# Optimization experiments

Hardware: AMD Instinct MI355X
Metric: run time of the kernel (lower is better)

## Reference

```python
import jax, jax.numpy as jnp
import numpy as np

N_NODES = 100000
N_EDGES = 20000
NNZ = 1600000
D_IN = 128
D_OUT = 128


def setup_inputs() -> dict:
    key = jax.random.key(0)
    k1, k2, k3, k4, k5 = jax.random.split(key, 5)
    x_0 = jax.random.normal(k1, (N_NODES, D_IN), dtype=jnp.float32)
    # Kaiming-uniform-ish linear params
    W = jax.random.normal(k2, (D_OUT, D_IN), dtype=jnp.float32) * (1.0 / np.sqrt(D_IN))
    b = jax.random.normal(k3, (D_OUT,), dtype=jnp.float32) * 0.01
    # COO nonzeros of incidence_1 [n_nodes, n_edges]
    node_idx = jax.random.randint(k4, (NNZ,), 0, N_NODES, dtype=jnp.int32)
    edge_idx = jax.random.randint(k5, (NNZ,), 0, N_EDGES, dtype=jnp.int32)
    return {"x_0": x_0, "W": W, "b": b, "node_idx": node_idx, "edge_idx": edge_idx}


def reference(x_0, W, b, node_idx, edge_idx):
    # Linear transform: h = x_0 @ W^T + b  -> [n_nodes, out_channels]
    h = jnp.einsum('nd,od->no', x_0, W) + b
    # Hop 1 (e_aggr='sum'): m_0_1[e] = sum_{n in edge e} h[n]   (B_1^T @ h)
    m_0_1 = jax.ops.segment_sum(h[node_idx], edge_idx, num_segments=N_EDGES)
    # Hop 2 (v_aggr='mean'): m_1_0[n] = mean_{e ni n} m_0_1[e]  (B_1 @ m_0_1, row-mean)
    msg_sum = jax.ops.segment_sum(m_0_1[edge_idx], node_idx, num_segments=N_NODES)
    deg = jax.ops.segment_sum(jnp.ones((node_idx.shape[0],), dtype=h.dtype),
                              node_idx, num_segments=N_NODES)
    m_1_0 = msg_sum / jnp.maximum(deg, 1.0)[:, None]  # empty rows -> 0, as torch reduce='mean'
    return h + m_1_0
```

## Files before the change

kernel.cpp:

```cpp
#include <hip/hip_runtime.h>
#include <hip/hip_bf16.h>
#include <stddef.h>

#define N_NODES 100000
#define N_EDGES 20000
#define NNZ     1600000
#define DIM     128

#define NCH     128
#define CHUNK   (NNZ / NCH)

#define EHIST_NB  NCH
#define NHIST_B0  EHIST_NB
#define GEMM_B0   (NHIST_B0 + NCH)
#define GEMM_NB   391
#define P1_NB     (GEMM_B0 + GEMM_NB)

#define EBL 79
#define NBL 391

typedef short          bf16x8 __attribute__((ext_vector_type(8)));
typedef unsigned short u16x8  __attribute__((ext_vector_type(8)));
typedef float          f32x4  __attribute__((ext_vector_type(4)));
typedef float          f32x8  __attribute__((ext_vector_type(8)));

__device__ __forceinline__ unsigned short f2bf(float f) {
  union { float f; unsigned u; } c; c.f = f;
  unsigned r = c.u + 0x7FFFu + ((c.u >> 16) & 1u);
  return (unsigned short)(r >> 16);
}

__device__ __forceinline__ f32x8 bf2f8(u16x8 v) {
  f32x8 r;
  #pragma unroll
  for (int i = 0; i < 8; ++i) {
    union { unsigned u; float f; } c; c.u = ((unsigned)v[i]) << 16;
    r[i] = c.f;
  }
  return r;
}

__global__ void convw_kernel(const float* __restrict__ W, unsigned short* __restrict__ Wb) {
  int i = blockIdx.x * 256 + threadIdx.x;
  if (i < DIM * DIM) Wb[i] = f2bf(W[i]);
}

__global__ __launch_bounds__(1024, 8) void p1_kernel(
    const float* __restrict__ x, const unsigned short* __restrict__ Wb,
    const float* __restrict__ bias, unsigned short* __restrict__ hb,
    const int* __restrict__ ni, const int* __restrict__ ei,
    unsigned short* __restrict__ bhE16, unsigned short* __restrict__ locE,
    unsigned char* __restrict__ bhN, unsigned char* __restrict__ locN) {
  __shared__ unsigned smem[12500];
  const int bid = blockIdx.x;

  if (bid < EHIST_NB) {
    const int cb = bid;
    for (int k = threadIdx.x; k < 10000; k += 1024) smem[k] = 0u;
    __syncthreads();
    const int base = cb * CHUNK;
    for (int i = base + threadIdx.x; i < base + CHUNK; i += 1024) {
      int e = ei[i];
      const int word  = e >> 1;
      const int shift = (e & 1) * 16;
      unsigned old = atomicAdd(&smem[word], 1u << shift);
      locE[i] = (unsigned short)((old >> shift) & 0xFFFFu);
    }
    __syncthreads();
    unsigned short* dst = bhE16 + (size_t)cb * N_EDGES;
    for (int e = threadIdx.x; e < N_EDGES; e += 1024)
      dst[e] = (unsigned short)((smem[e >> 1] >> ((e & 1) * 16)) & 0xFFFFu);
  } else if (bid < GEMM_B0) {
    const int cb = bid - NHIST_B0;
    for (int k = threadIdx.x; k < 12500; k += 1024) smem[k] = 0u;
    __syncthreads();
    const int base = cb * CHUNK;
    for (int i = base + threadIdx.x; i < base + CHUNK; i += 1024) {
      int n = ni[i];
      const int word  = n >> 3;
      const int shift = (n & 7) * 4;
      unsigned old = atomicAdd(&smem[word], 1u << shift);
      locN[i] = (unsigned char)((old >> shift) & 15u);
    }
    __syncthreads();
    unsigned char* dst = bhN + (size_t)cb * N_NODES;
    for (int k = threadIdx.x; k < N_NODES; k += 1024)
      dst[k] = (unsigned char)((smem[k >> 3] >> ((k & 7) * 4)) & 15u);
  } else {
    const int wid = threadIdx.x >> 6;
    const int l   = threadIdx.x & 63;
    const int n0  = ((bid - GEMM_B0) * 16 + wid) * 16;
    if (n0 >= N_NODES) return;
    const int r  = l & 15;
    const int kg = l >> 4;

    bf16x8 a[4];
    {
      const float* xr = x + (size_t)(n0 + r) * DIM + kg * 8;
      #pragma unroll
      for (int kc = 0; kc < 4; ++kc) {
        const float4* p = reinterpret_cast<const float4*>(xr + kc * 32);
        float4 f0 = p[0], f1 = p[1];
        bf16x8 av;
        av[0]=(short)f2bf(f0.x); av[1]=(short)f2bf(f0.y); av[2]=(short)f2bf(f0.z); av[3]=(short)f2bf(f0.w);
        av[4]=(short)f2bf(f1.x); av[5]=(short)f2bf(f1.y); av[6]=(short)f2bf(f1.z); av[7]=(short)f2bf(f1.w);
        a[kc] = av;
      }
    }

    f32x4 acc[8];
    #pragma unroll
    for (int ot = 0; ot < 8; ++ot) acc[ot] = (f32x4){0.f, 0.f, 0.f, 0.f};

    #pragma unroll
    for (int ot = 0; ot < 8; ++ot) {
      const unsigned short* wr = Wb + (size_t)(r * 8 + ot) * DIM + kg * 8;
      #pragma unroll
      for (int kc = 0; kc < 4; ++kc) {
        bf16x8 bfrag = *reinterpret_cast<const bf16x8*>(wr + kc * 32);
        acc[ot] = __builtin_amdgcn_mfma_f32_16x16x32_bf16(a[kc], bfrag, acc[ot], 0, 0, 0);
      }
    }

    float bv[8];
    {
      const float4* bp = reinterpret_cast<const float4*>(bias + r * 8);
      float4 b0 = bp[0], b1 = bp[1];
      bv[0]=b0.x; bv[1]=b0.y; bv[2]=b0.z; bv[3]=b0.w;
      bv[4]=b1.x; bv[5]=b1.y; bv[6]=b1.z; bv[7]=b1.w;
    }

    #pragma unroll
    for (int j = 0; j < 4; ++j) {
      const int row = kg * 4 + j;
      u16x8 hv;
      #pragma unroll
      for (int ot = 0; ot < 8; ++ot) hv[ot] = f2bf(acc[ot][j] + bv[ot]);
      *reinterpret_cast<u16x8*>(&hb[(size_t)(n0 + row) * DIM + r * 8]) = hv;
    }
  }
}

__global__ __launch_bounds__(256) void scansA_kernel(
    unsigned short* __restrict__ bhE16, unsigned char* __restrict__ bhN,
    int* __restrict__ off_e, int* __restrict__ off_n,
    int* __restrict__ ebs, int* __restrict__ nbs) {
  __shared__ int lds[256];
  const int tx  = threadIdx.x;
  const int bid = blockIdx.x;
  int v;
  if (bid < EBL) {
    const int e = bid * 256 + tx;
    v = 0;
    if (e < N_EDGES) {
      unsigned short* p = bhE16 + e;
      int s = 0;
      #pragma unroll 8
      for (int b = 0; b < NCH; ++b) {
        int t = p[(size_t)b * N_EDGES];
        p[(size_t)b * N_EDGES] = (unsigned short)s;
        s += t;
      }
      v = s;
    }
  } else {
    const int k = (bid - EBL) * 256 + tx;
    v = 0;
    if (k < N_NODES) {
      unsigned char* p = bhN + k;
      int s = 0;
      #pragma unroll 8
      for (int b = 0; b < NCH; ++b) {
        int t = p[(size_t)b * N_NODES];
        p[(size_t)b * N_NODES] = (unsigned char)s;
        s += t;
      }
      v = s;
    }
  }
  int xv = v;
  lds[tx] = xv;
  __syncthreads();
  for (int off = 1; off < 256; off <<= 1) {
    int t = (tx >= off) ? lds[tx - off] : 0;
    __syncthreads();
    xv += t;
    lds[tx] = xv;
    __syncthreads();
  }
  if (bid < EBL) {
    const int e = bid * 256 + tx;
    if (e < N_EDGES) off_e[e] = xv - v;
    if (tx == 255) ebs[bid] = xv;
  } else {
    const int k = (bid - EBL) * 256 + tx;
    if (k < N_NODES) off_n[k] = xv - v;
    if (tx == 255) nbs[bid - EBL] = xv;
  }
}

__global__ __launch_bounds__(512) void scansB_kernel(int* __restrict__ ebs,
                                                     int* __restrict__ nbs) {
  __shared__ int lds[512];
  const int tx = threadIdx.x;
  int* a = (blockIdx.x == 0) ? ebs : nbs;
  const int m = (blockIdx.x == 0) ? EBL : NBL;
  int v = (tx < m) ? a[tx] : 0;
  int xv = v;
  lds[tx] = xv;
  __syncthreads();
  for (int off = 1; off < 512; off <<= 1) {
    int t = (tx >= off) ? lds[tx - off] : 0;
    __syncthreads();
    xv += t;
    lds[tx] = xv;
    __syncthreads();
  }
  if (tx < m) a[tx] = xv - v;
}

__global__ __launch_bounds__(256) void scansC_kernel(
    int* __restrict__ off_e, int* __restrict__ off_n,
    const int* __restrict__ ebs, const int* __restrict__ nbs) {
  const int tx  = threadIdx.x;
  const int bid = blockIdx.x;
  if (bid < EBL) {
    const int e = bid * 256 + tx;
    if (e < N_EDGES) off_e[e] += ebs[bid];
  } else {
    const int k = (bid - EBL) * 256 + tx;
    if (k < N_NODES) off_n[k] += nbs[bid - EBL];
  }
}

__global__ void scatter_kernel(const int* __restrict__ ni, const int* __restrict__ ei,
                               const int* __restrict__ off_n, const int* __restrict__ off_e,
                               const unsigned short* __restrict__ bhE16,
                               const unsigned char* __restrict__ bhN,
                               const unsigned short* __restrict__ locE,
                               const unsigned char* __restrict__ locN,
                               int* __restrict__ csr_e2n, int* __restrict__ csr_n2e) {
  int i = blockIdx.x * 256 + threadIdx.x;
  if (i < NNZ) {
    int n = ni[i], e = ei[i];
    int blk = i / CHUNK;
    csr_e2n[off_e[e] + (int)bhE16[(size_t)blk * N_EDGES + e] + (int)locE[i]] = n;
    csr_n2e[off_n[n] + (int)bhN[(size_t)blk * N_NODES + n] + (int)locN[i]] = e;
  }
}

__global__ __launch_bounds__(256) void hop1_kernel(
    const unsigned short* __restrict__ hb, const int* __restrict__ off_e,
    const int* __restrict__ csr_e2n, unsigned short* __restrict__ m01b) {
  const int e = blockIdx.x * 16 + (threadIdx.x >> 4);
  const int l = threadIdx.x & 15;
  if (e >= N_EDGES) return;
  const int s   = off_e[e];
  const int end = (e == N_EDGES - 1) ? NNZ : off_e[e + 1];

  f32x8 a0 = (f32x8){0.f,0.f,0.f,0.f,0.f,0.f,0.f,0.f};
  f32x8 a1 = a0, a2 = a0, a3 = a0;
  int j = s;
  for (; j + 3 < end; j += 4) {
    const int n0 = csr_e2n[j + 0];
    const int n1 = csr_e2n[j + 1];
    const int n2 = csr_e2n[j + 2];
    const int n3 = csr_e2n[j + 3];
    u16x8 v0 = *reinterpret_cast<const u16x8*>(&hb[(size_t)n0 * DIM + l * 8]);
    u16x8 v1 = *reinterpret_cast<const u16x8*>(&hb[(size_t)n1 * DIM + l * 8]);
    u16x8 v2 = *reinterpret_cast<const u16x8*>(&hb[(size_t)n2 * DIM + l * 8]);
    u16x8 v3 = *reinterpret_cast<const u16x8*>(&hb[(size_t)n3 * DIM + l * 8]);
    a0 += bf2f8(v0); a1 += bf2f8(v1); a2 += bf2f8(v2); a3 += bf2f8(v3);
  }
  for (; j < end; ++j) {
    const int n = csr_e2n[j];
    a0 += bf2f8(*reinterpret_cast<const u16x8*>(&hb[(size_t)n * DIM + l * 8]));
  }
  f32x8 r = (a0 + a1) + (a2 + a3);
  u16x8 o;
  #pragma unroll
  for (int i = 0; i < 8; ++i) o[i] = f2bf(r[i]);
  *reinterpret_cast<u16x8*>(&m01b[(size_t)e * DIM + l * 8]) = o;
}

__global__ __launch_bounds__(256) void hop2_kernel(
    const unsigned short* __restrict__ hb, const int* __restrict__ off_n,
    const int* __restrict__ csr_n2e, const unsigned short* __restrict__ m01b,
    float* __restrict__ out) {
  const int n = blockIdx.x * 16 + (threadIdx.x >> 4);
  const int l = threadIdx.x & 15;
  if (n >= N_NODES) return;
  const int s   = off_n[n];
  const int end = (n == N_NODES - 1) ? NNZ : off_n[n + 1];
  const int cnt = end - s;

  f32x8 a0 = (f32x8){0.f,0.f,0.f,0.f,0.f,0.f,0.f,0.f};
  f32x8 a1 = a0;
  int j = s;
  for (; j + 1 < end; j += 2) {
    const int e0 = csr_n2e[j + 0];
    const int e1 = csr_n2e[j + 1];
    u16x8 v0 = *reinterpret_cast<const u16x8*>(&m01b[(size_t)e0 * DIM + l * 8]);
    u16x8 v1 = *reinterpret_cast<const u16x8*>(&m01b[(size_t)e1 * DIM + l * 8]);
    a0 += bf2f8(v0); a1 += bf2f8(v1);
  }
  if (j < end) {
    const int e = csr_n2e[j];
    a0 += bf2f8(*reinterpret_cast<const u16x8*>(&m01b[(size_t)e * DIM + l * 8]));
  }
  f32x8 r  = a0 + a1;
  f32x8 hv = bf2f8(*reinterpret_cast<const u16x8*>(&hb[(size_t)n * DIM + l * 8]));
  const float inv = 1.0f / (float)(cnt > 0 ? cnt : 1);
  f32x8 o = hv + r * inv;
  float* op = &out[(size_t)n * DIM + l * 8];
  *reinterpret_cast<f32x4*>(op)     = (f32x4){o[0], o[1], o[2], o[3]};
  *reinterpret_cast<f32x4*>(op + 4) = (f32x4){o[4], o[5], o[6], o[7]};
}

extern "C" void kernel_launch(void* const* d_in, const int* in_sizes, int n_in,
                              void* d_out, int out_size, void* d_ws, size_t ws_size,
                              hipStream_t stream) {
  const float* x    = (const float*)d_in[0];
  const float* W    = (const float*)d_in[1];
  const float* bias = (const float*)d_in[2];
  const int*   ni   = (const int*)d_in[3];
  const int*   ei   = (const int*)d_in[4];
  float* out = (float*)d_out;

  char* ws = (char*)d_ws;
  size_t o = 0;
  auto carve = [&](size_t bytes) -> char* {
    char* p = ws + o;
    o = (o + bytes + 255) & ~(size_t)255;
    return p;
  };
  unsigned short* hb      = (unsigned short*)carve((size_t)N_NODES * DIM * 2);
  unsigned short* m01b    = (unsigned short*)carve((size_t)N_EDGES * DIM * 2);
  int*            csr_e2n = (int*)           carve((size_t)NNZ * 4);
  int*            csr_n2e = (int*)           carve((size_t)NNZ * 4);
  unsigned short* locE    = (unsigned short*)carve((size_t)NNZ * 2);
  unsigned char*  locN    = (unsigned char*) carve((size_t)NNZ);
  unsigned short* Wb      = (unsigned short*)carve((size_t)DIM * DIM * 2);
  unsigned short* bhE16   = (unsigned short*)carve((size_t)NCH * N_EDGES * 2);
  unsigned char*  bhN     = (unsigned char*) carve((size_t)NCH * N_NODES);
  int*            off_n   = (int*)           carve((size_t)N_NODES * 4);
  int*            off_e   = (int*)           carve((size_t)N_EDGES * 4);
  int*            ebs     = (int*)           carve(EBL * 4);
  int*            nbs     = (int*)           carve(NBL * 4);
  (void)ws_size; (void)in_sizes; (void)n_in; (void)out_size;

  convw_kernel<<<(DIM * DIM + 255) / 256, 256, 0, stream>>>(W, Wb);

  p1_kernel<<<P1_NB, 1024, 0, stream>>>(x, Wb, bias, hb, ni, ei,
                                        bhE16, locE, bhN, locN);

  scansA_kernel<<<EBL + NBL, 256, 0, stream>>>(bhE16, bhN, off_e, off_n, ebs, nbs);
  scansB_kernel<<<2, 512, 0, stream>>>(ebs, nbs);
  scansC_kernel<<<EBL + NBL, 256, 0, stream>>>(off_e, off_n, ebs, nbs);

  scatter_kernel<<<NNZ / 256, 256, 0, stream>>>(ni, ei, off_n, off_e,
                                                bhE16, bhN, locE, locN,
                                                csr_e2n, csr_n2e);

  hop1_kernel<<<(N_EDGES + 15) / 16, 256, 0, stream>>>(hb, off_e, csr_e2n, m01b);
  hop2_kernel<<<(N_NODES + 15) / 16, 256, 0, stream>>>(hb, off_n, csr_n2e, m01b, out);
}
```

Measured before the change: 226.4 us.

## Split CSR scatter and overlap node-side scatter with hop1 via dynamic work queues

Splits the combined scatter into an edge-side scatter, then launches one kernel whose first blocks run hop1 and whose remaining blocks build the node-to-edge CSR, so the two independent stages can run at the same time. Hop1 and hop2 now have each block own a segment of edges or nodes, and each 16-lane group pulls its next item from a shared-memory atomic counter to balance uneven degrees. This adds an extra launch plus shared atomics and shuffles per item, and the heterogeneous blocks in the fused kernel can compete for resources.

New measurement: 236.2 us. +4.3%, slower.

```diff
diff --git a/kernel.cpp b/kernel.cpp
--- a/kernel.cpp
+++ b/kernel.cpp
@@ -18,6 +18,13 @@
 
 #define EBL 79
 #define NBL 391
+
+#define H1_SEG 32
+#define H1_NB  (N_EDGES / H1_SEG)
+#define SCN_NB (NNZ / 256)
+#define P2_NB  (H1_NB + SCN_NB)
+#define H2_SEG 64
+#define H2_NB  ((N_NODES + H2_SEG - 1) / H2_SEG)
 
 typedef short          bf16x8 __attribute__((ext_vector_type(8)));
 typedef unsigned short u16x8  __attribute__((ext_vector_type(8)));
@@ -233,88 +240,119 @@
   }
 }
 
-__global__ void scatter_kernel(const int* __restrict__ ni, const int* __restrict__ ei,
-                               const int* __restrict__ off_n, const int* __restrict__ off_e,
-                               const unsigned short* __restrict__ bhE16,
-                               const unsigned char* __restrict__ bhN,
-                               const unsigned short* __restrict__ locE,
-                               const unsigned char* __restrict__ locN,
-                               int* __restrict__ csr_e2n, int* __restrict__ csr_n2e) {
+__global__ __launch_bounds__(256) void scatterE_kernel(
+    const int* __restrict__ ni, const int* __restrict__ ei,
+    const int* __restrict__ off_e,
+    const unsigned short* __restrict__ bhE16,
+    const unsigned short* __restrict__ locE,
+    int* __restrict__ csr_e2n) {
   int i = blockIdx.x * 256 + threadIdx.x;
   if (i < NNZ) {
-    int n = ni[i], e = ei[i];
+    int e = ei[i];
     int blk = i / CHUNK;
-    csr_e2n[off_e[e] + (int)bhE16[(size_t)blk * N_EDGES + e] + (int)locE[i]] = n;
-    csr_n2e[off_n[n] + (int)bhN[(size_t)blk * N_NODES + n] + (int)locN[i]] = e;
-  }
-}
-
-__global__ __launch_bounds__(256) void hop1_kernel(
+    csr_e2n[off_e[e] + (int)bhE16[(size_t)blk * N_EDGES + e] + (int)locE[i]] = ni[i];
+  }
+}
+
+__global__ __launch_bounds__(256) void p2_kernel(
     const unsigned short* __restrict__ hb, const int* __restrict__ off_e,
-    const int* __restrict__ csr_e2n, unsigned short* __restrict__ m01b) {
-  const int e = blockIdx.x * 16 + (threadIdx.x >> 4);
-  const int l = threadIdx.x & 15;
-  if (e >= N_EDGES) return;
-  const int s   = off_e[e];
-  const int end = (e == N_EDGES - 1) ? NNZ : off_e[e + 1];
-
-  f32x8 a0 = (f32x8){0.f,0.f,0.f,0.f,0.f,0.f,0.f,0.f};
-  f32x8 a1 = a0, a2 = a0, a3 = a0;
-  int j = s;
-  for (; j + 3 < end; j += 4) {
-    const int n0 = csr_e2n[j + 0];
-    const int n1 = csr_e2n[j + 1];
-    const int n2 = csr_e2n[j + 2];
-    const int n3 = csr_e2n[j + 3];
-    u16x8 v0 = *reinterpret_cast<const u16x8*>(&hb[(size_t)n0 * DIM + l * 8]);
-    u16x8 v1 = *reinterpret_cast<const u16x8*>(&hb[(size_t)n1 * DIM + l * 8]);
-    u16x8 v2 = *reinterpret_cast<const u16x8*>(&hb[(size_t)n2 * DIM + l * 8]);
-    u16x8 v3 = *reinterpret_cast<const u16x8*>(&hb[(size_t)n3 * DIM + l * 8]);
-    a0 += bf2f8(v0); a1 += bf2f8(v1); a2 += bf2f8(v2); a3 += bf2f8(v3);
-  }
-  for (; j < end; ++j) {
-    const int n = csr_e2n[j];
-    a0 += bf2f8(*reinterpret_cast<const u16x8*>(&hb[(size_t)n * DIM + l * 8]));
-  }
-  f32x8 r = (a0 + a1) + (a2 + a3);
-  u16x8 o;
-  #pragma unroll
-  for (int i = 0; i < 8; ++i) o[i] = f2bf(r[i]);
-  *reinterpret_cast<u16x8*>(&m01b[(size_t)e * DIM + l * 8]) = o;
+    const int* __restrict__ csr_e2n, unsigned short* __restrict__ m01b,
+    const int* __restrict__ ni, const int* __restrict__ ei,
+    const int* __restrict__ off_n,
+    const unsigned char* __restrict__ bhN, const unsigned char* __restrict__ locN,
+    int* __restrict__ csr_n2e) {
+  const int bid = blockIdx.x;
+  if (bid < H1_NB) {
+    __shared__ int ctr;
+    const int g = threadIdx.x >> 4;
+    const int l = threadIdx.x & 15;
+    if (threadIdx.x == 0) ctr = 16;
+    __syncthreads();
+    int eloc = g;
+    while (eloc < H1_SEG) {
+      const int e = bid * H1_SEG + eloc;
+      const int s   = off_e[e];
+      const int end = (e == N_EDGES - 1) ? NNZ : off_e[e + 1];
+      f32x8 a0 = (f32x8){0.f,0.f,0.f,0.f,0.f,0.f,0.f,0.f};
+      f32x8 a1 = a0, a2 = a0, a3 = a0;
+      int j = s;
+      for (; j + 3 < end; j += 4) {
+        const int n0 = csr_e2n[j + 0];
+        const int n1 = csr_e2n[j + 1];
+        const int n2 = csr_e2n[j + 2];
+        const int n3 = csr_e2n[j + 3];
+        u16x8 v0 = *reinterpret_cast<const u16x8*>(&hb[(size_t)n0 * DIM + l * 8]);
+        u16x8 v1 = *reinterpret_cast<const u16x8*>(&hb[(size_t)n1 * DIM + l * 8]);
+        u16x8 v2 = *reinterpret_cast<const u16x8*>(&hb[(size_t)n2 * DIM + l * 8]);
+        u16x8 v3 = *reinterpret_cast<const u16x8*>(&hb[(size_t)n3 * DIM + l * 8]);
+        a0 += bf2f8(v0); a1 += bf2f8(v1); a2 += bf2f8(v2); a3 += bf2f8(v3);
+      }
+      for (; j < end; ++j) {
+        const int n = csr_e2n[j];
+        a0 += bf2f8(*reinterpret_cast<const u16x8*>(&hb[(size_t)n * DIM + l * 8]));
+      }
+      f32x8 r = (a0 + a1) + (a2 + a3);
+      u16x8 o;
+      #pragma unroll
+      for (int m = 0; m < 8; ++m) o[m] = f2bf(r[m]);
+      *reinterpret_cast<u16x8*>(&m01b[(size_t)e * DIM + l * 8]) = o;
+      int nxt = 0;
+      if (l == 0) nxt = atomicAdd(&ctr, 1);
+      eloc = __shfl(nxt, threadIdx.x & 48);
+    }
+  } else {
+    const int i = (bid - H1_NB) * 256 + threadIdx.x;
+    if (i < NNZ) {
+      int n = ni[i];
+      int blk = i / CHUNK;
+      csr_n2e[off_n[n] + (int)bhN[(size_t)blk * N_NODES + n] + (int)locN[i]] = ei[i];
+    }
+  }
 }
 
 __global__ __launch_bounds__(256) void hop2_kernel(
     const unsigned short* __restrict__ hb, const int* __restrict__ off_n,
     const int* __restrict__ csr_n2e, const unsigned short* __restrict__ m01b,
     float* __restrict__ out) {
-  const int n = blockIdx.x * 16 + (threadIdx.x >> 4);
+  __shared__ int ctr;
+  const int g = threadIdx.x >> 4;
   const int l = threadIdx.x & 15;
-  if (n >= N_NODES) return;
-  const int s   = off_n[n];
-  const int end = (n == N_NODES - 1) ? NNZ : off_n[n + 1];
-  const int cnt = end - s;
-
-  f32x8 a0 = (f32x8){0.f,0.f,0.f,0.f,0.f,0.f,0.f,0.f};
-  f32x8 a1 = a0;
-  int j = s;
-  for (; j + 1 < end; j += 2) {
-    const int e0 = csr_n2e[j + 0];
-    const int e1 = csr_n2e[j + 1];
-    u16x8 v0 = *reinterpret_cast<const u16x8*>(&m01b[(size_t)e0 * DIM + l * 8]);
-    u16x8 v1 = *reinterpret_cast<const u16x8*>(&m01b[(size_t)e1 * DIM + l * 8]);
-    a0 += bf2f8(v0); a1 += bf2f8(v1);
-  }
-  if (j < end) {
-    const int e = csr_n2e[j];
-    a0 += bf2f8(*reinterpret_cast<const u16x8*>(&m01b[(size_t)e * DIM + l * 8]));
-  }
-  f32x8 r  = a0 + a1;
-  f32x8 hv = bf2f8(*reinterpret_cast<const u16x8*>(&hb[(size_t)n * DIM + l * 8]));
-  const float inv = 1.0f / (float)(cnt > 0 ? cnt : 1);
-  f32x8 o = hv + r * inv;
-  float* op = &out[(size_t)n * DIM + l * 8];
-  *reinterpret_cast<f32x4*>(op)     = (f32x4){o[0], o[1], o[2], o[3]};
-  *reinterpret_cast<f32x4*>(op + 4) = (f32x4){o[4], o[5], o[6], o[7]};
+  if (threadIdx.x == 0) ctr = 16;
+  __syncthreads();
+  const int bid = blockIdx.x;
+  int nloc = g;
+  while (nloc < H2_SEG) {
+    const int n = bid * H2_SEG + nloc;
+    if (n < N_NODES) {
+      const int s   = off_n[n];
+      const int end = (n == N_NODES - 1) ? NNZ : off_n[n + 1];
+      const int cnt = end - s;
+      f32x8 a0 = (f32x8){0.f,0.f,0.f,0.f,0.f,0.f,0.f,0.f};
+      f32x8 a1 = a0;
+      int j = s;
+      for (; j + 1 < end; j += 2) {
+        const int e0 = csr_n2e[j + 0];
+        const int e1 = csr_n2e[j + 1];
+        u16x8 v0 = *reinterpret_cast<const u16x8*>(&m01b[(size_t)e0 * DIM + l * 8]);
+        u16x8 v1 = *reinterpret_cast<const u16x8*>(&m01b[(size_t)e1 * DIM + l * 8]);
+        a0 += bf2f8(v0); a1 += bf2f8(v1);
+      }
+      if (j < end) {
+        const int e = csr_n2e[j];
+        a0 += bf2f8(*reinterpret_cast<const u16x8*>(&m01b[(size_t)e * DIM + l * 8]));
+      }
+      f32x8 r  = a0 + a1;
+      f32x8 hv = bf2f8(*reinterpret_cast<const u16x8*>(&hb[(size_t)n * DIM + l * 8]));
+      const float inv = 1.0f / (float)(cnt > 0 ? cnt : 1);
+      f32x8 o = hv + r * inv;
+      float* op = &out[(size_t)n * DIM + l * 8];
+      *reinterpret_cast<f32x4*>(op)     = (f32x4){o[0], o[1], o[2], o[3]};
+      *reinterpret_cast<f32x4*>(op + 4) = (f32x4){o[4], o[5], o[6], o[7]};
+    }
+    int nxt = 0;
+    if (l == 0) nxt = atomicAdd(&ctr, 1);
+    nloc = __shfl(nxt, threadIdx.x & 48);
+  }
 }
 
 extern "C" void kernel_launch(void* const* d_in, const int* in_sizes, int n_in,
@@ -358,10 +396,10 @@
   scansB_kernel<<<2, 512, 0, stream>>>(ebs, nbs);
   scansC_kernel<<<EBL + NBL, 256, 0, stream>>>(off_e, off_n, ebs, nbs);
 
-  scatter_kernel<<<NNZ / 256, 256, 0, stream>>>(ni, ei, off_n, off_e,
-                                                bhE16, bhN, locE, locN,
-                                                csr_e2n, csr_n2e);
-
-  hop1_kernel<<<(N_EDGES + 15) / 16, 256, 0, stream>>>(hb, off_e, csr_e2n, m01b);
-  hop2_kernel<<<(N_NODES + 15) / 16, 256, 0, stream>>>(hb, off_n, csr_n2e, m01b, out);
-}
+  scatterE_kernel<<<SCN_NB, 256, 0, stream>>>(ni, ei, off_e, bhE16, locE, csr_e2n);
+
+  p2_kernel<<<P2_NB, 256, 0, stream>>>(hb, off_e, csr_e2n, m01b,
+                                       ni, ei, off_n, bhN, locN, csr_n2e);
+
+  hop2_kernel<<<H2_NB, 256, 0, stream>>>(hb, off_n, csr_n2e, m01b, out);
+}
```
